# Kernel optimization log

Measured on AMD Instinct MI355X. Metric: run time of the kernel, lower is better.

Reference implementation:

```python
import jax, jax.numpy as jnp
import numpy as np

D, H = 2048, 16
Q_RANK, KV_RANK = 1536, 512
NOPE, ROPE_D, V_D = 128, 64, 128
QK_D = NOPE + ROPE_D  # 192
S, B = 2048, 1
THETA = 10000.0
EPS = 1e-5


def rmsnorm(x, w, eps=EPS):
    return x * jax.lax.rsqrt(jnp.mean(x * x, -1, keepdims=True) + eps) * w


def rope_cos_sin(s, d, theta=THETA):
    inv = 1.0 / (theta ** (jnp.arange(0, d, 2, dtype=jnp.float32) / d))
    f = jnp.arange(s, dtype=jnp.float32)[:, None] * inv[None, :]  # [s, d//2]
    emb = jnp.concatenate([f, f], -1)  # [s, d]
    return jnp.cos(emb), jnp.sin(emb)


def apply_rope(x, cos, sin):
    # DeepSeek-V3 variant: de-interleave consecutive pairs into [even | odd] halves first
    b, h, s, d = x.shape
    x = x.reshape(b, h, s, d // 2, 2).transpose(0, 1, 2, 4, 3).reshape(b, h, s, d)
    x1, x2 = jnp.split(x, 2, -1)
    rot = jnp.concatenate([-x2, x1], -1)
    return x * cos + rot * sin


def setup_inputs() -> dict:
    key = jax.random.key(0)
    ks = jax.random.split(key, 10)
    s = 0.02
    return {
        "x": jax.random.normal(ks[0], (S, B, D), jnp.float32),
        "norm1_w": jnp.ones((D,), jnp.float32),
        "q_a_w": jax.random.normal(ks[1], (D, Q_RANK), jnp.float32) * s,
        "q_a_ln_w": jnp.ones((Q_RANK,), jnp.float32),
        "q_b_w": jax.random.normal(ks[2], (Q_RANK, H * QK_D), jnp.float32) * s,
        "kv_a_w": jax.random.normal(ks[3], (D, KV_RANK + ROPE_D), jnp.float32) * s,
        "kv_a_ln_w": jnp.ones((KV_RANK,), jnp.float32),
        "kv_b_w": jax.random.normal(ks[4], (KV_RANK, H * (NOPE + V_D)), jnp.float32) * s,
        "o_w": jax.random.normal(ks[5], (H * V_D, D), jnp.float32) * s,
        "norm2_w": jnp.ones((D,), jnp.float32),
        "ffn_w1": jax.random.normal(ks[6], (D, 4 * D), jnp.float32) * s,
        "ffn_b1": jnp.zeros((4 * D,), jnp.float32),
        "ffn_w2": jax.random.normal(ks[7], (4 * D, D), jnp.float32) * s,
        "ffn_b2": jnp.zeros((D,), jnp.float32),
    }


def reference(x, norm1_w, q_a_w, q_a_ln_w, q_b_w, kv_a_w, kv_a_ln_w, kv_b_w, o_w,
              norm2_w, ffn_w1, ffn_b1, ffn_w2, ffn_b2):
    # x: [S, B, D] (block transposes to [B, S, D] before MLA)
    hs = jnp.swapaxes(rmsnorm(x, norm1_w), 0, 1)  # [B, S, D]
    b, s, _ = hs.shape

    # --- MLA: low-rank Q and KV with decoupled RoPE ---
    q = rmsnorm(hs @ q_a_w, q_a_ln_w) @ q_b_w                    # [B, S, H*192]
    q = q.reshape(b, s, H, QK_D).transpose(0, 2, 1, 3)           # [B, H, S, 192]
    q_nope, q_pe = q[..., :NOPE], q[..., NOPE:]

    kv_a = hs @ kv_a_w                                           # [B, S, 576]
    c_kv, k_pe = kv_a[..., :KV_RANK], kv_a[..., KV_RANK:]        # [B,S,512], [B,S,64]
    kv = rmsnorm(c_kv, kv_a_ln_w) @ kv_b_w                       # [B, S, H*256]
    kv = kv.reshape(b, s, H, NOPE + V_D).transpose(0, 2, 1, 3)   # [B, H, S, 256]
    k_nope, v = kv[..., :NOPE], kv[..., NOPE:]

    cos, sin = rope_cos_sin(s, ROPE_D)
    q_pe = apply_rope(q_pe, cos, sin)                            # [B, H, S, 64]
    k_pe = apply_rope(k_pe[:, None, :, :], cos, sin)             # [B, 1, S, 64]

    q_full = jnp.concatenate([q_nope, q_pe], -1)                 # [B, H, S, 192]
    k_full = jnp.concatenate([k_nope, jnp.broadcast_to(k_pe, (b, H, s, ROPE_D))], -1)

    scores = jnp.einsum('bhqd,bhkd->bhqk', q_full, k_full) * (1.0 / np.sqrt(QK_D))
    causal = jnp.tril(jnp.ones((s, s), bool))
    scores = jnp.where(causal, scores, jnp.finfo(scores.dtype).min)
    attn = jax.nn.softmax(scores, -1)
    out = jnp.einsum('bhqk,bhkd->bhqd', attn, v)                 # [B, H, S, 128]
    out = out.transpose(0, 2, 1, 3).reshape(b, s, H * V_D) @ o_w # [B, S, D]

    x = x + jnp.swapaxes(out, 0, 1)                              # residual, back to [S,B,D]

    # --- FFN (exact GELU) ---
    h2 = rmsnorm(x, norm2_w)
    ffn = jax.nn.gelu(h2 @ ffn_w1 + ffn_b1, approximate=False) @ ffn_w2 + ffn_b2
    return x + ffn
```

## Files before the change

### kernel.cpp

```cpp
#include <hip/hip_runtime.h>
#include <hip/hip_bf16.h>

typedef __hip_bfloat16 bf16;
using bf16x8 = __attribute__((ext_vector_type(8))) __bf16;
using f32x4  = __attribute__((ext_vector_type(4))) float;

#define S_   2048
#define D_   2048
#define H_   16
#define QR_  1536
#define KVR_ 512
#define NOPE_ 128
#define ROPE_ 64
#define VD_  128
#define QKD_ 192
#define EPS_ 1e-5f
#define QKVN 2112

#define GLDS16(g, l) \
    __builtin_amdgcn_global_load_lds((const __attribute__((address_space(1))) void*)(g), \
                                     (__attribute__((address_space(3))) void*)(l), 16, 0, 0)

__global__ __launch_bounds__(256) void gemm_k(
    const bf16* __restrict__ A, const bf16* __restrict__ BT, void* __restrict__ Cv,
    const float* __restrict__ bias, const float* __restrict__ res,
    int M, int N, int K, int lda, int ldb, int ldc,
    long long strideA, long long strideB, long long strideC,
    int mode, int causal, int ksplit, int kchunk)
{
    int bn = blockIdx.x, bm = blockIdx.y;
    int bzC = blockIdx.z;
    int bz = bzC, kc = 0;
    if (ksplit > 1) { kc = bzC % ksplit; bz = bzC / ksplit; }
    if (causal == 1 && bn > bm) return;
    A  += (size_t)bz * strideA;
    BT += (size_t)bz * strideB;

    int k_end = K;
    if (causal == 2) { int kl = (bm + 1) * 128; if (kl < k_end) k_end = kl; }
    int k_begin = kc * kchunk;
    if (k_begin + kchunk < k_end) k_end = k_begin + kchunk;
    if (k_begin >= k_end) return;
    int nIter = (k_end - k_begin) >> 5;

    __shared__ bf16 sA[2 * 128 * 32];
    __shared__ bf16 sB[2 * 128 * 32];

    int tid  = threadIdx.x;
    int lane = tid & 63, wave = tid >> 6;
    int wr = wave >> 1, wc = wave & 1;
    int fr = lane & 15, fq = lane >> 4;

    int row0 = bm * 128, col0 = bn * 128;

    int srow = wave * 16 + (lane >> 2);
    int sko  = (lane & 3) * 8;
    const bf16* ga0 = A + (size_t)(row0 + srow) * lda + sko;
    const bf16* ga1 = ga0 + (size_t)64 * lda;
    int bn0 = col0 + srow;      if (bn0 > N - 1) bn0 = N - 1;
    int bn1 = col0 + srow + 64; if (bn1 > N - 1) bn1 = N - 1;
    const bf16* gb0 = BT + (size_t)bn0 * ldb + sko;
    const bf16* gb1 = BT + (size_t)bn1 * ldb + sko;
    bf16* lA0 = &sA[(wave * 16) * 32];
    bf16* lA1 = &sA[(64 + wave * 16) * 32];
    bf16* lB0 = &sB[(wave * 16) * 32];
    bf16* lB1 = &sB[(64 + wave * 16) * 32];

#define STAGE(buf, k0) do {                       \
        GLDS16(ga0 + (k0), lA0 + (buf) * 4096);   \
        GLDS16(ga1 + (k0), lA1 + (buf) * 4096);   \
        GLDS16(gb0 + (k0), lB0 + (buf) * 4096);   \
        GLDS16(gb1 + (k0), lB1 + (buf) * 4096);   \
    } while (0)

    f32x4 acc[4][4] = {};

#define COMPUTE(buf) do {                                                           \
        bf16x8 af[4], bv[4];                                                        \
        _Pragma("unroll")                                                           \
        for (int i = 0; i < 4; ++i)                                                 \
            af[i] = *(const bf16x8*)&sA[(buf)*4096 + (wr*64 + i*16 + fr)*32 + fq*8];\
        _Pragma("unroll")                                                           \
        for (int j = 0; j < 4; ++j)                                                 \
            bv[j] = *(const bf16x8*)&sB[(buf)*4096 + (wc*64 + j*16 + fr)*32 + fq*8];\
        _Pragma("unroll")                                                           \
        for (int i = 0; i < 4; ++i)                                                 \
            _Pragma("unroll")                                                       \
            for (int j = 0; j < 4; ++j)                                             \
                acc[i][j] = __builtin_amdgcn_mfma_f32_16x16x32_bf16(af[i], bv[j], acc[i][j], 0, 0, 0); \
    } while (0)

    STAGE(0, k_begin);
    for (int it = 0; it < nIter; it += 2) {
        __syncthreads();
        if (it + 1 < nIter) STAGE(1, k_begin + (it + 1) * 32);
        COMPUTE(0);
        if (it + 1 < nIter) {
            __syncthreads();
            if (it + 2 < nIter) STAGE(0, k_begin + (it + 2) * 32);
            COMPUTE(1);
        }
    }
#undef STAGE
#undef COMPUTE

    #pragma unroll
    for (int i = 0; i < 4; ++i) {
        #pragma unroll
        for (int j = 0; j < 4; ++j) {
            int gc = col0 + wc*64 + j*16 + fr;
            if (gc >= N) continue;
            #pragma unroll
            for (int r = 0; r < 4; ++r) {
                int gr = row0 + wr*64 + i*16 + fq*4 + r;
                float v = acc[i][j][r];
                size_t off = (size_t)bzC * strideC + (size_t)gr * ldc + gc;
                if (mode == 0 || mode == 6) {
                    ((float*)Cv)[off] = v;
                } else if (mode == 1) {
                    ((bf16*)Cv)[off] = __float2bfloat16(v);
                } else if (mode == 2) {
                    ((float*)Cv)[off] = v + res[(size_t)gr * ldc + gc];
                } else if (mode == 3) {
                    float t = v + bias[gc];
                    t = 0.5f * t * (1.0f + erff(t * 0.70710678118654752f));
                    ((bf16*)Cv)[off] = __float2bfloat16(t);
                } else {
                    ((float*)Cv)[off] = v + bias[gc] + res[(size_t)gr * ldc + gc];
                }
            }
        }
    }
}

__global__ __launch_bounds__(256) void red_k(const float* __restrict__ part,
        long long pstride4, int nch, const float* __restrict__ res,
        const float* __restrict__ bias, long long cols4,
        float* __restrict__ dstF, bf16* __restrict__ dstB, long long n4)
{
    long long i = (long long)blockIdx.x * 256 + threadIdx.x;
    long long stride = (long long)gridDim.x * 256;
    for (; i < n4; i += stride) {
        float4 v = ((const float4*)part)[i];
        for (int k = 1; k < nch; ++k) {
            float4 p = ((const float4*)part)[i + k * pstride4];
            v.x += p.x; v.y += p.y; v.z += p.z; v.w += p.w;
        }
        if (res) {
            float4 rr = ((const float4*)res)[i];
            v.x += rr.x; v.y += rr.y; v.z += rr.z; v.w += rr.w;
        }
        if (bias) {
            float4 b = ((const float4*)bias)[i % cols4];
            v.x += b.x; v.y += b.y; v.z += b.z; v.w += b.w;
        }
        if (dstB) {
            ushort4 o;
            bf16 t0 = __float2bfloat16(v.x); o.x = *(unsigned short*)&t0;
            bf16 t1 = __float2bfloat16(v.y); o.y = *(unsigned short*)&t1;
            bf16 t2 = __float2bfloat16(v.z); o.z = *(unsigned short*)&t2;
            bf16 t3 = __float2bfloat16(v.w); o.w = *(unsigned short*)&t3;
            ((ushort4*)dstB)[i] = o;
        } else {
            ((float4*)dstF)[i] = v;
        }
    }
}

__global__ __launch_bounds__(128) void pv_red(const float* __restrict__ part,
                                              bf16* __restrict__ ao, int grp)
{
    int r = blockIdx.x, head = blockIdx.y, d = threadIdx.x;
    int nv = ((r >> 7) + 4) >> 2;
    const float* p = part + ((size_t)head * 4) * S_ * VD_ + (size_t)r * VD_ + d;
    float s = 0.f;
    for (int k = 0; k < nv; ++k) s += p[(size_t)k * S_ * VD_];
    ao[(size_t)r * (H_ * VD_) + grp * 1024 + head * VD_ + d] = __float2bfloat16(s);
}

__global__ __launch_bounds__(256) void transpose_w(const float* __restrict__ in,
                                                   bf16* __restrict__ out, int R, int C)
{
    __shared__ float t[32][33];
    int c0 = blockIdx.x * 32, r0 = blockIdx.y * 32;
    int tx = threadIdx.x, ty = threadIdx.y;
    for (int j = ty; j < 32; j += 8) {
        int r = r0 + j, c = c0 + tx;
        t[j][tx] = (r < R && c < C) ? in[(size_t)r * C + c] : 0.f;
    }
    __syncthreads();
    for (int j = ty; j < 32; j += 8) {
        int c = c0 + j, r = r0 + tx;
        if (c < C && r < R) out[(size_t)c * R + r] = __float2bfloat16(t[tx][j]);
    }
}

__global__ __launch_bounds__(256) void transpose_v(const bf16* __restrict__ kv,
                                                   bf16* __restrict__ vT)
{
    __shared__ bf16 t[32][33];
    int h = blockIdx.z;
    int d0 = blockIdx.x * 32, s0 = blockIdx.y * 32;
    int tx = threadIdx.x, ty = threadIdx.y;
    for (int j = ty; j < 32; j += 8)
        t[j][tx] = kv[(size_t)(s0 + j) * (H_*256) + h*256 + 128 + d0 + tx];
    __syncthreads();
    for (int j = ty; j < 32; j += 8)
        vT[((size_t)h * VD_ + d0 + j) * S_ + s0 + tx] = t[tx][j];
}

__global__ __launch_bounds__(256) void rmsnorm_k(const float* __restrict__ in,
                                                 const float* __restrict__ w,
                                                 bf16* __restrict__ out,
                                                 int cols, int istride, int ostride)
{
    int row = blockIdx.x, tid = threadIdx.x;
    const float* ip = in + (size_t)row * istride;
    bf16* op = out + (size_t)row * ostride;
    float ss = 0.f;
    for (int c = tid; c < cols; c += 256) { float v = ip[c]; ss = fmaf(v, v, ss); }
    for (int o = 32; o > 0; o >>= 1) ss += __shfl_down(ss, o, 64);
    __shared__ float red[4];
    __shared__ float s_sc;
    int wave = tid >> 6, lane = tid & 63;
    if (lane == 0) red[wave] = ss;
    __syncthreads();
    if (tid == 0) s_sc = rsqrtf((red[0]+red[1]+red[2]+red[3]) / (float)cols + EPS_);
    __syncthreads();
    float sc = s_sc;
    for (int c = tid; c < cols; c += 256)
        op[c] = __float2bfloat16(ip[c] * sc * w[c]);
}

#define ROPE_LC 0.28782313662425575f

__global__ __launch_bounds__(192) void build_q(const bf16* __restrict__ q,
                                               bf16* __restrict__ qf)
{
    int s = blockIdx.x, h = blockIdx.y, t = threadIdx.x;
    const float scale = 0.07216878364870323f;
    const bf16* src = q + (size_t)s * (H_*QKD_) + h * QKD_;
    bf16* dst = qf + ((size_t)h * S_ + s) * QKD_;
    if (t < NOPE_) {
        dst[t] = __float2bfloat16(__bfloat162float(src[t]) * scale);
    } else {
        int i = (t - NOPE_) & 31;
        bool hi = (t - NOPE_) >= 32;
        float a = __bfloat162float(src[NOPE_ + 2*i]);
        float b = __bfloat162float(src[NOPE_ + 2*i + 1]);
        float inv = __expf(-(float)i * ROPE_LC);
        float f = (float)s * inv, c, sn;
        sincosf(f, &sn, &c);
        float v = hi ? (b * c + a * sn) : (a * c - b * sn);
        dst[t] = __float2bfloat16(v * scale);
    }
}

__global__ __launch_bounds__(192) void build_k(const bf16* __restrict__ kv,
                                               const float* __restrict__ qakva32,
                                               bf16* __restrict__ kf)
{
    int s = blockIdx.x, h = blockIdx.y, t = threadIdx.x;
    const bf16* src = kv + (size_t)s * (H_*256) + h * 256;
    bf16* dst = kf + ((size_t)h * S_ + s) * QKD_;
    if (t < NOPE_) {
        dst[t] = src[t];
    } else {
        int i = (t - NOPE_) & 31;
        bool hi = (t - NOPE_) >= 32;
        const float* pe = qakva32 + (size_t)s * QKVN + (QR_ + KVR_);
        float a = pe[2*i], b = pe[2*i + 1];
        float inv = __expf(-(float)i * ROPE_LC);
        float f = (float)s * inv, c, sn;
        sincosf(f, &sn, &c);
        dst[t] = __float2bfloat16(hi ? (b * c + a * sn) : (a * c - b * sn));
    }
}

__global__ __launch_bounds__(256) void softmax_k(bf16* __restrict__ Sc)
{
    int q = blockIdx.x, h = blockIdx.y;
    bf16* row = Sc + ((size_t)h * S_ + q) * S_;
    int n = q + 1;
    int klim = ((q >> 7) + 1) << 7;
    int tid = threadIdx.x, lane = tid & 63, wave = tid >> 6;
    __shared__ float red[4];
    __shared__ float bc;

    float v[8];
    #pragma unroll
    for (int k = 0; k < 8; ++k) {
        int c = tid + k * 256;
        v[k] = (c < n) ? __bfloat162float(row[c]) : -3.0e38f;
    }
    float mx = v[0];
    #pragma unroll
    for (int k = 1; k < 8; ++k) mx = fmaxf(mx, v[k]);
    for (int o = 32; o > 0; o >>= 1) mx = fmaxf(mx, __shfl_down(mx, o, 64));
    if (lane == 0) red[wave] = mx;
    __syncthreads();
    if (tid == 0) bc = fmaxf(fmaxf(red[0], red[1]), fmaxf(red[2], red[3]));
    __syncthreads();
    float m = bc;
    float sum = 0.f;
    #pragma unroll
    for (int k = 0; k < 8; ++k) {
        int c = tid + k * 256;
        v[k] = (c < n) ? __expf(v[k] - m) : 0.f;
        sum += v[k];
    }
    for (int o = 32; o > 0; o >>= 1) sum += __shfl_down(sum, o, 64);
    __syncthreads();
    if (lane == 0) red[wave] = sum;
    __syncthreads();
    if (tid == 0) bc = 1.0f / (red[0] + red[1] + red[2] + red[3]);
    __syncthreads();
    float inv = bc;
    #pragma unroll
    for (int k = 0; k < 8; ++k) {
        int c = tid + k * 256;
        if (c < klim) row[c] = __float2bfloat16(c < n ? v[k] * inv : 0.f);
    }
}

static inline void gemm(hipStream_t st, const bf16* A, const bf16* BT, void* C,
                        const float* bias, const float* res,
                        int M, int N, int K, int lda, int ldb, int ldc,
                        long long sA, long long sB, long long sC,
                        int batch, int mode, int causal, int ksplit = 1, int kchunk = 0)
{
    if (kchunk == 0) kchunk = K;
    dim3 g((N + 127) / 128, M / 128, batch * ksplit);
    gemm_k<<<g, 256, 0, st>>>(A, BT, C, bias, res, M, N, K, lda, ldb, ldc,
                              sA, sB, sC, mode, causal, ksplit, kchunk);
}

static inline void transw(hipStream_t st, const float* in, bf16* out, int R, int C)
{
    dim3 g((C + 31) / 32, (R + 31) / 32);
    transpose_w<<<g, dim3(32, 8), 0, st>>>(in, out, R, C);
}

extern "C" void kernel_launch(void* const* d_in, const int* in_sizes, int n_in,
                              void* d_out, int out_size, void* d_ws, size_t ws_size,
                              hipStream_t stream)
{
    const float* x        = (const float*)d_in[0];
    const float* norm1_w  = (const float*)d_in[1];
    const float* q_a_w    = (const float*)d_in[2];
    const float* q_a_ln_w = (const float*)d_in[3];
    const float* q_b_w    = (const float*)d_in[4];
    const float* kv_a_w   = (const float*)d_in[5];
    const float* kv_a_ln_w= (const float*)d_in[6];
    const float* kv_b_w   = (const float*)d_in[7];
    const float* o_w      = (const float*)d_in[8];
    const float* norm2_w  = (const float*)d_in[9];
    const float* ffn_w1   = (const float*)d_in[10];
    const float* ffn_b1   = (const float*)d_in[11];
    const float* ffn_w2   = (const float*)d_in[12];
    const float* ffn_b2   = (const float*)d_in[13];
    float* out = (float*)d_out;

    size_t off = 0;
    auto alloc = [&](size_t bytes) -> void* {
        void* p = (char*)d_ws + off;
        off += (bytes + 255) & ~(size_t)255;
        return p;
    };
    bf16*  hs     = (bf16*) alloc((size_t)S_*D_*2);
    bf16*  wqakvT = (bf16*) alloc((size_t)QKVN*D_*2);
    bf16*  wqbT   = (bf16*) alloc((size_t)(H_*QKD_)*QR_*2);
    bf16*  wkvbT  = (bf16*) alloc((size_t)(H_*(NOPE_+VD_))*KVR_*2);
    bf16*  woT    = (bf16*) alloc((size_t)D_*(H_*VD_)*2);
    bf16*  wf1T   = (bf16*) alloc((size_t)(4*D_)*D_*2);
    bf16*  wf2T   = (bf16*) alloc((size_t)D_*(4*D_)*2);
    float* qakva32= (float*)alloc((size_t)S_*QKVN*4);
    bf16*  qln    = (bf16*) alloc((size_t)S_*QR_*2);
    bf16*  kvln   = (bf16*) alloc((size_t)S_*KVR_*2);
    bf16*  qb     = (bf16*) alloc((size_t)S_*H_*QKD_*2);
    bf16*  kvb    = (bf16*) alloc((size_t)S_*H_*(NOPE_+VD_)*2);
    bf16*  qf     = (bf16*) alloc((size_t)H_*S_*QKD_*2);
    bf16*  kf     = (bf16*) alloc((size_t)H_*S_*QKD_*2);
    bf16*  vT     = (bf16*) alloc((size_t)H_*VD_*S_*2);
    bf16*  Sc     = (bf16*) alloc((size_t)8*S_*S_*2);
    float* qakvaP = (float*)Sc;
    float* qbP    = (float*)Sc;
    float* pvP    = (float*)qakva32;
    float* oP     = (float*)qf;
    float* f2P    = (float*)qf;
    float* x2     = qakva32;
    bf16*  h2     = qb;
    bf16*  ao     = kvb;
    bf16*  a1     = Sc;

    transw(stream, q_a_w,  wqakvT,                    D_,  QR_);
    transw(stream, kv_a_w, wqakvT + (size_t)QR_ * D_, D_,  KVR_+ROPE_);
    transw(stream, q_b_w,  wqbT,  QR_, H_*QKD_);
    transw(stream, kv_b_w, wkvbT, KVR_, H_*(NOPE_+VD_));
    transw(stream, o_w,    woT,   H_*VD_, D_);
    transw(stream, ffn_w1, wf1T,  D_,  4*D_);
    transw(stream, ffn_w2, wf2T,  4*D_, D_);

    rmsnorm_k<<<S_, 256, 0, stream>>>(x, norm1_w, hs, D_, D_, D_);

    gemm(stream, hs, wqakvT, qakvaP, nullptr, nullptr, S_, QKVN, D_, D_, D_, QKVN,
         0, 0, (long long)S_*QKVN, 1, 6, 0, 2, 1024);
    red_k<<<1024, 256, 0, stream>>>(qakvaP, (long long)S_*QKVN/4, 2, nullptr, nullptr, 1,
                                    qakva32, nullptr, (long long)S_*QKVN/4);

    rmsnorm_k<<<S_, 256, 0, stream>>>(qakva32, q_a_ln_w, qln, QR_, QKVN, QR_);
    gemm(stream, qln, wqbT, qbP, nullptr, nullptr, S_, H_*QKD_, QR_, QR_, QR_, H_*QKD_,
         0, 0, (long long)S_*(H_*QKD_), 1, 6, 0, 2, 768);
    red_k<<<1024, 256, 0, stream>>>(qbP, (long long)S_*(H_*QKD_)/4, 2, nullptr, nullptr, 1,
                                    nullptr, qb, (long long)S_*(H_*QKD_)/4);

    rmsnorm_k<<<S_, 256, 0, stream>>>(qakva32 + QR_, kv_a_ln_w, kvln, KVR_, QKVN, KVR_);
    gemm(stream, kvln, wkvbT, kvb, nullptr, nullptr, S_, H_*(NOPE_+VD_), KVR_,
         KVR_, KVR_, H_*(NOPE_+VD_), 0, 0, 0, 1, 1, 0);

    build_q<<<dim3(S_, H_), 192, 0, stream>>>(qb, qf);
    build_k<<<dim3(S_, H_), 192, 0, stream>>>(kvb, qakva32, kf);
    transpose_v<<<dim3(VD_/32, S_/32, H_), dim3(32, 8), 0, stream>>>(kvb, vT);

    for (int g = 0; g < 2; ++g) {
        const bf16* qfg = qf + (size_t)g * 8 * S_ * QKD_;
        const bf16* kfg = kf + (size_t)g * 8 * S_ * QKD_;
        const bf16* vTg = vT + (size_t)g * 8 * VD_ * S_;
        gemm(stream, qfg, kfg, Sc, nullptr, nullptr,
             S_, S_, QKD_, QKD_, QKD_, S_,
             (long long)S_*QKD_, (long long)S_*QKD_, (long long)S_*S_, 8, 1, 1);
        softmax_k<<<dim3(S_, 8), 256, 0, stream>>>(Sc);
        gemm(stream, Sc, vTg, pvP, nullptr, nullptr,
             S_, VD_, S_, S_, S_, VD_,
             (long long)S_*S_, (long long)VD_*S_, (long long)S_*VD_, 8, 6, 2, 4, 512);
        pv_red<<<dim3(S_, 8), 128, 0, stream>>>(pvP, ao, g);
    }

    gemm(stream, ao, woT, oP, nullptr, nullptr, S_, D_, H_*VD_, H_*VD_, H_*VD_, D_,
         0, 0, (long long)S_*D_, 1, 6, 0, 2, 1024);
    red_k<<<1024, 256, 0, stream>>>(oP, (long long)S_*D_/4, 2, x, nullptr, 1,
                                    x2, nullptr, (long long)S_*D_/4);

    rmsnorm_k<<<S_, 256, 0, stream>>>(x2, norm2_w, h2, D_, D_, D_);
    gemm(stream, h2, wf1T, a1, ffn_b1, nullptr, S_, 4*D_, D_, D_, D_, 4*D_,
         0, 0, 0, 1, 3, 0);
    gemm(stream, a1, wf2T, f2P, nullptr, nullptr, S_, D_, 4*D_, 4*D_, 4*D_, D_,
         0, 0, (long long)S_*D_, 1, 6, 0, 2, 4096);
    red_k<<<1024, 256, 0, stream>>>(f2P, (long long)S_*D_/4, 2, x2, ffn_b2, D_/4,
                                    out, nullptr, (long long)S_*D_/4);
}
```

Measured before the change: 1.069 ms.

## Triple-buffer GEMM LDS pipeline with partial vmcnt waits

Moves the GEMM main loop from double to triple buffering in LDS, so loads run two K-steps ahead of compute. Raw s_waitcnt vmcnt(4) plus s_barrier replaces __syncthreads, so each iteration waits only for the older stage's loads while the newer prefetch stays in flight. This aims to hide global-to-LDS latency better. In exchange, LDS use rises by half, which can lower occupancy, and the hand-written waitcnt counting depends on the compiler not reordering or adding other vector memory ops.

```diff
diff --git a/kernel.cpp b/kernel.cpp
--- a/kernel.cpp
+++ b/kernel.cpp
@@ -21,6 +21,9 @@
     __builtin_amdgcn_global_load_lds((const __attribute__((address_space(1))) void*)(g), \
                                      (__attribute__((address_space(3))) void*)(l), 16, 0, 0)
 
+#define PIPE_WAIT4 asm volatile("s_waitcnt vmcnt(4)\n\ts_barrier" ::: "memory")
+#define PIPE_WAIT0 asm volatile("s_waitcnt vmcnt(0)\n\ts_barrier" ::: "memory")
+
 __global__ __launch_bounds__(256) void gemm_k(
     const bf16* __restrict__ A, const bf16* __restrict__ BT, void* __restrict__ Cv,
     const float* __restrict__ bias, const float* __restrict__ res,
@@ -43,8 +46,8 @@
     if (k_begin >= k_end) return;
     int nIter = (k_end - k_begin) >> 5;
 
-    __shared__ bf16 sA[2 * 128 * 32];
-    __shared__ bf16 sB[2 * 128 * 32];
+    __shared__ bf16 sA[3 * 128 * 32];
+    __shared__ bf16 sB[3 * 128 * 32];
 
     int tid  = threadIdx.x;
     int lane = tid & 63, wave = tid >> 6;
@@ -66,23 +69,23 @@
     bf16* lB0 = &sB[(wave * 16) * 32];
     bf16* lB1 = &sB[(64 + wave * 16) * 32];
 
-#define STAGE(buf, k0) do {                       \
-        GLDS16(ga0 + (k0), lA0 + (buf) * 4096);   \
-        GLDS16(ga1 + (k0), lA1 + (buf) * 4096);   \
-        GLDS16(gb0 + (k0), lB0 + (buf) * 4096);   \
-        GLDS16(gb1 + (k0), lB1 + (buf) * 4096);   \
+#define STAGE(ofs, k0) do {                  \
+        GLDS16(ga0 + (k0), lA0 + (ofs));     \
+        GLDS16(ga1 + (k0), lA1 + (ofs));     \
+        GLDS16(gb0 + (k0), lB0 + (ofs));     \
+        GLDS16(gb1 + (k0), lB1 + (ofs));     \
     } while (0)
 
     f32x4 acc[4][4] = {};
 
-#define COMPUTE(buf) do {                                                           \
+#define COMPUTE(ofs) do {                                                           \
         bf16x8 af[4], bv[4];                                                        \
         _Pragma("unroll")                                                           \
         for (int i = 0; i < 4; ++i)                                                 \
-            af[i] = *(const bf16x8*)&sA[(buf)*4096 + (wr*64 + i*16 + fr)*32 + fq*8];\
+            af[i] = *(const bf16x8*)&sA[(ofs) + (wr*64 + i*16 + fr)*32 + fq*8];     \
         _Pragma("unroll")                                                           \
         for (int j = 0; j < 4; ++j)                                                 \
-            bv[j] = *(const bf16x8*)&sB[(buf)*4096 + (wc*64 + j*16 + fr)*32 + fq*8];\
+            bv[j] = *(const bf16x8*)&sB[(ofs) + (wc*64 + j*16 + fr)*32 + fq*8];     \
         _Pragma("unroll")                                                           \
         for (int i = 0; i < 4; ++i)                                                 \
             _Pragma("unroll")                                                       \
@@ -91,16 +94,19 @@
     } while (0)
 
     STAGE(0, k_begin);
-    for (int it = 0; it < nIter; it += 2) {
-        __syncthreads();
-        if (it + 1 < nIter) STAGE(1, k_begin + (it + 1) * 32);
-        COMPUTE(0);
-        if (it + 1 < nIter) {
-            __syncthreads();
-            if (it + 2 < nIter) STAGE(0, k_begin + (it + 2) * 32);
-            COMPUTE(1);
-        }
-    }
+    if (nIter > 1) STAGE(4096, k_begin + 32);
+
+    int curo = 0, pfo = 8192;
+    int it = 0;
+    for (; it < nIter - 1; ++it) {
+        PIPE_WAIT4;
+        if (it + 2 < nIter) STAGE(pfo, k_begin + (it + 2) * 32);
+        COMPUTE(curo);
+        curo += 4096; if (curo == 12288) curo = 0;
+        pfo  += 4096; if (pfo  == 12288) pfo  = 0;
+    }
+    PIPE_WAIT0;
+    COMPUTE(curo);
 #undef STAGE
 #undef COMPUTE
 
```

Result: faster. 970.8 us (-9.2%).
